# Kernel tuning notes

Hardware: AMD Instinct MI355X
Metric: run time of the kernel (lower is better)

The kernel has to match this reference:

```python
import jax, jax.numpy as jnp
import numpy as np

D_MODEL = 2048
N_HEADS = 16
HEAD_DIM = D_MODEL // N_HEADS  # 128
B, T = 2, 1024
XL_LEN = 1024


def setup_inputs() -> dict:
    key = jax.random.key(0)
    ks = jax.random.split(key, 8)
    # rotary angles for head_dim/2 pairs (llama-style)
    inv_freq = 1.0 / (10000.0 ** (jnp.arange(0, HEAD_DIM, 2, dtype=jnp.float32) / HEAD_DIM))
    t = jnp.arange(T, dtype=jnp.float32)
    freqs = jnp.outer(t, inv_freq)  # [T, HEAD_DIM//2]
    return {
        "x": jax.random.normal(ks[0], (B, T, D_MODEL), dtype=jnp.float32),
        "cos": jnp.cos(freqs),
        "sin": jnp.sin(freqs),
        "k_xl": jax.random.normal(ks[1], (B, XL_LEN, D_MODEL), dtype=jnp.float32),
        "v_xl": jax.random.normal(ks[2], (B, XL_LEN, D_MODEL), dtype=jnp.float32),
        "pos_emb": jax.random.normal(ks[3], (XL_LEN, D_MODEL), dtype=jnp.float32) * 0.02,
        "w_qkv": jax.random.normal(ks[4], (3 * D_MODEL, D_MODEL), dtype=jnp.float32) * 0.02,
        "w_proj": jax.random.normal(ks[5], (D_MODEL, D_MODEL), dtype=jnp.float32) * 0.02,
        "is_causal": 0,
    }


def _apply_rope(x, cos, sin):
    # x: [B, T, H, hd]; cos/sin: [T, hd//2]
    xr = x.reshape(*x.shape[:-1], HEAD_DIM // 2, 2)
    x1, x2 = xr[..., 0], xr[..., 1]
    c = cos[None, :, None, :]
    s = sin[None, :, None, :]
    o1 = x1 * c - x2 * s
    o2 = x1 * s + x2 * c
    return jnp.stack([o1, o2], axis=-1).reshape(x.shape)


def reference(x, cos, sin, k_xl, v_xl, pos_emb, w_qkv, w_proj, is_causal):
    Bq, Tq, C = x.shape
    H, hd = N_HEADS, HEAD_DIM
    qkv = jnp.einsum('btc,fc->btf', x, w_qkv)  # fused QKV projection
    q, k, v = jnp.split(qkv, 3, axis=-1)
    # add learned XL positional embedding to cached keys (self.k_xl += emb(arange))
    k_xl = k_xl + pos_emb[None, :, :]
    q = q.reshape(Bq, Tq, H, hd)
    k = k.reshape(Bq, -1, H, hd)
    v = v.reshape(Bq, -1, H, hd)
    q = _apply_rope(q, cos, sin)
    k = _apply_rope(k, cos, sin)
    q = q.transpose(0, 2, 1, 3)  # [B,H,T,hd]
    k = k.transpose(0, 2, 1, 3)
    v = v.transpose(0, 2, 1, 3)
    k_xl_h = k_xl.reshape(Bq, -1, H, hd).transpose(0, 2, 1, 3)
    v_xl_h = v_xl.reshape(Bq, -1, H, hd).transpose(0, 2, 1, 3)
    k_full = jnp.concatenate([k_xl_h, k], axis=-2)  # [B,H,XL+T,hd]
    v_full = jnp.concatenate([v_xl_h, v], axis=-2)
    scale = 1.0 / jnp.sqrt(jnp.asarray(hd, dtype=q.dtype))
    scores = jnp.einsum('bhqd,bhkd->bhqk', q, k_full) * scale
    if is_causal:
        Kv = k_full.shape[-2]
        qi = jnp.arange(Tq)[:, None]
        ki = jnp.arange(Kv)[None, :]
        scores = jnp.where(ki <= qi + (Kv - Tq), scores, jnp.finfo(scores.dtype).min)
    attn = jax.nn.softmax(scores, axis=-1)
    y = jnp.einsum('bhqk,bhkd->bhqd', attn, v_full)
    y = y.transpose(0, 2, 1, 3).reshape(Bq, Tq, C)
    return jnp.einsum('btc,oc->bto', y, w_proj)
```

## Files before the change

### kernel.cpp

```cpp
#include <hip/hip_runtime.h>
#include <stdint.h>

typedef unsigned short u16;
typedef __attribute__((ext_vector_type(4))) float f32x4;
typedef __attribute__((ext_vector_type(8))) short bf16x8;
typedef __attribute__((ext_vector_type(4))) uint32_t u32x4;

#define D_MODEL 2048
#define NHEADS 16
#define HD 128
#define BSZ 2
#define TQ 1024
#define XL 1024
#define KVLEN 2048

__device__ __forceinline__ float b2f(u16 u) {
  union { uint32_t i; float f; } x; x.i = ((uint32_t)u) << 16; return x.f;
}
__device__ __forceinline__ u16 f2b(float f) {
  union { float f; uint32_t i; } x; x.f = f;
  uint32_t r = x.i + 0x7FFFu + ((x.i >> 16) & 1u);
  return (u16)(r >> 16);
}

union U4 { u32x4 u; u16 s[8]; };

__device__ __forceinline__ void async_copy16(const u16* g, u16* l) {
  __builtin_amdgcn_global_load_lds((__attribute__((address_space(1))) void*)g,
                                   (__attribute__((address_space(3))) void*)l,
                                   16, 0, 0);
}

__device__ __forceinline__ float rmax16(float v) {
  v = fmaxf(v, __shfl_xor(v, 1));
  v = fmaxf(v, __shfl_xor(v, 2));
  v = fmaxf(v, __shfl_xor(v, 4));
  v = fmaxf(v, __shfl_xor(v, 8));
  return v;
}
__device__ __forceinline__ float rsum16(float v) {
  v += __shfl_xor(v, 1);
  v += __shfl_xor(v, 2);
  v += __shfl_xor(v, 4);
  v += __shfl_xor(v, 8);
  return v;
}

struct PrefF32 {
  f32x4 lo, hi;
  __device__ __forceinline__ void load(const float* base, size_t off) {
    lo = *(const f32x4*)(base + off);
    hi = *(const f32x4*)(base + off + 4);
  }
  __device__ __forceinline__ u32x4 pack() const {
    U4 o;
    o.s[0] = f2b(lo[0]); o.s[1] = f2b(lo[1]); o.s[2] = f2b(lo[2]); o.s[3] = f2b(lo[3]);
    o.s[4] = f2b(hi[0]); o.s[5] = f2b(hi[1]); o.s[6] = f2b(hi[2]); o.s[7] = f2b(hi[3]);
    return o.u;
  }
};

__global__ __launch_bounds__(256, 4) void cvt_bf16(
    const float* __restrict__ src, u16* __restrict__ dst)
{
  const size_t id = (size_t)blockIdx.x * 256 + threadIdx.x;
  PrefF32 p; p.load(src, id * 8);
  *(u32x4*)&dst[id * 8] = p.pack();
}

template <bool AF32, bool BF32, bool CSPLIT>
__global__ __launch_bounds__(256, 2) void gemm_bt(
    const void* __restrict__ Av, const void* __restrict__ Bv,
    void* __restrict__ C0, void* __restrict__ C1, void* __restrict__ C2,
    int M, int N, int K)
{
  __shared__ u16 sA[128 * 32];
  __shared__ u16 sB[128 * 32];
  const int tid  = threadIdx.x;
  const int lane = tid & 63;
  const int wave = tid >> 6;
  const int quad = lane >> 4;
  const int mcol = lane & 15;
  const int wm = (wave >> 1) * 64;
  const int wn = (wave & 1) * 64;
  const int bm = blockIdx.y * 128;
  const int bnE = blockIdx.x * 128;

  f32x4 acc[4][4] = {};

  const int c0 = tid, c1 = tid + 256;
  size_t a0 = (size_t)(bm + (c0 >> 2)) * K + (c0 & 3) * 8;
  size_t a1 = (size_t)(bm + (c1 >> 2)) * K + (c1 & 3) * 8;
  size_t b0 = (size_t)(bnE + (c0 >> 2)) * K + (c0 & 3) * 8;
  size_t b1 = (size_t)(bnE + (c1 >> 2)) * K + (c1 & 3) * 8;

  PrefF32 pa0, pa1, pb0, pb1;
  if (AF32) { pa0.load((const float*)Av, a0); pa1.load((const float*)Av, a1); }
  if (BF32) { pb0.load((const float*)Bv, b0); pb1.load((const float*)Bv, b1); }

  const int nk = K >> 5;
  for (int kk = 0; kk < nk; ++kk) {
    if (!AF32) {
      async_copy16((const u16*)Av + a0, &sA[c0 * 8]);
      async_copy16((const u16*)Av + a1, &sA[c1 * 8]);
      a0 += 32; a1 += 32;
    } else {
      *(u32x4*)&sA[c0 * 8] = pa0.pack();
      *(u32x4*)&sA[c1 * 8] = pa1.pack();
    }
    if (!BF32) {
      async_copy16((const u16*)Bv + b0, &sB[c0 * 8]);
      async_copy16((const u16*)Bv + b1, &sB[c1 * 8]);
      b0 += 32; b1 += 32;
    } else {
      *(u32x4*)&sB[c0 * 8] = pb0.pack();
      *(u32x4*)&sB[c1 * 8] = pb1.pack();
    }
    __syncthreads();
    if (kk + 1 < nk) {
      if (AF32) { a0 += 32; a1 += 32; pa0.load((const float*)Av, a0); pa1.load((const float*)Av, a1); }
      if (BF32) { b0 += 32; b1 += 32; pb0.load((const float*)Bv, b0); pb1.load((const float*)Bv, b1); }
    }
    bf16x8 af[4], bff[4];
#pragma unroll
    for (int i = 0; i < 4; ++i) {
      af[i]  = *(const bf16x8*)&sA[(wm + i * 16 + mcol) * 32 + quad * 8];
      bff[i] = *(const bf16x8*)&sB[(wn + i * 16 + mcol) * 32 + quad * 8];
    }
#pragma unroll
    for (int i = 0; i < 4; ++i)
#pragma unroll
      for (int j = 0; j < 4; ++j)
        acc[i][j] = __builtin_amdgcn_mfma_f32_16x16x32_bf16(af[i], bff[j], acc[i][j], 0, 0, 0);
    __syncthreads();
  }

  if (CSPLIT) {
    const int sel = bnE >> 11;
    u16* Cp = (u16*)(sel == 0 ? C0 : (sel == 1 ? C1 : C2));
    const int bnl = (bnE & 2047) + wn;
#pragma unroll
    for (int i = 0; i < 4; ++i)
#pragma unroll
      for (int r = 0; r < 4; ++r) {
        const size_t base = (size_t)(bm + wm + i * 16 + quad * 4 + r) * 2048 + bnl;
#pragma unroll
        for (int j = 0; j < 4; ++j)
          Cp[base + j * 16 + mcol] = f2b(acc[i][j][r]);
      }
  } else {
    float* Cp = (float*)C0;
#pragma unroll
    for (int i = 0; i < 4; ++i)
#pragma unroll
      for (int r = 0; r < 4; ++r) {
        const size_t base = (size_t)(bm + wm + i * 16 + quad * 4 + r) * N + bnE + wn;
#pragma unroll
        for (int j = 0; j < 4; ++j)
          Cp[base + j * 16 + mcol] = acc[i][j][r];
      }
  }
}

__global__ __launch_bounds__(256, 4) void prep_k(
    const float* __restrict__ kxl, const float* __restrict__ pos,
    const u16* __restrict__ kbuf, const float* __restrict__ cosw,
    const float* __restrict__ sinw, u16* __restrict__ kfull)
{
  const int id = blockIdx.x * 256 + threadIdx.x;
  const int dc = id & 15;
  const int kv = (id >> 4) & 2047;
  const int bh = id >> 15;
  const int b = bh >> 4, h = bh & 15;
  const int d0 = dc * 8;
  U4 o;
  if (kv < XL) {
    const float* kp = kxl + ((size_t)b * XL + kv) * D_MODEL + h * HD + d0;
    const float* pp = pos + (size_t)kv * D_MODEL + h * HD + d0;
    f32x4 kl = *(const f32x4*)kp, kh = *(const f32x4*)(kp + 4);
    f32x4 pl = *(const f32x4*)pp, ph = *(const f32x4*)(pp + 4);
#pragma unroll
    for (int p = 0; p < 4; ++p) {
      o.s[p]     = f2b(kl[p] + pl[p]);
      o.s[4 + p] = f2b(kh[p] + ph[p]);
    }
  } else {
    const int tq = kv - XL;
    U4 kv_;
    kv_.u = *(const u32x4*)(kbuf + ((size_t)b * TQ + tq) * D_MODEL + h * HD + d0);
    f32x4 cv = *(const f32x4*)(cosw + tq * 64 + (d0 >> 1));
    f32x4 sv = *(const f32x4*)(sinw + tq * 64 + (d0 >> 1));
#pragma unroll
    for (int p = 0; p < 4; ++p) {
      const float e = b2f(kv_.s[2 * p]), od = b2f(kv_.s[2 * p + 1]);
      o.s[2 * p]     = f2b(e * cv[p] - od * sv[p]);
      o.s[2 * p + 1] = f2b(e * sv[p] + od * cv[p]);
    }
  }
  *(u32x4*)&kfull[((size_t)bh * KVLEN + kv) * HD + d0] = o.u;
}

__global__ __launch_bounds__(256, 4) void transpose_v(
    const float* __restrict__ v_xl, const u16* __restrict__ vbuf, u16* __restrict__ vt)
{
  __shared__ u16 tile[64 * 72];
  const int tid = threadIdx.x;
  const int kv0 = blockIdx.x * 64;
  const int d0  = blockIdx.y * 64;
  const int bh  = blockIdx.z;
  const int b = bh >> 4, h = bh & 15;
#pragma unroll
  for (int j = 0; j < 2; ++j) {
    const int id = tid + 256 * j;
    const int kr = id >> 3, dq = (id & 7) * 8;
    const int kvg = kv0 + kr;
    if (kvg < XL) {
      const float* src = v_xl + ((size_t)b * XL + kvg) * D_MODEL + h * HD + d0 + dq;
      PrefF32 p; p.load(src, 0);
      *(u32x4*)&tile[kr * 72 + dq] = p.pack();
    } else {
      const u16* src = vbuf + ((size_t)b * TQ + (kvg - XL)) * D_MODEL + h * HD + d0 + dq;
      *(u32x4*)&tile[kr * 72 + dq] = *(const u32x4*)src;
    }
  }
  __syncthreads();
#pragma unroll
  for (int j = 0; j < 2; ++j) {
    const int id = tid + 256 * j;
    const int dr = id >> 3, kq = (id & 7) * 8;
    U4 ov;
#pragma unroll
    for (int i = 0; i < 8; ++i) ov.s[i] = tile[(kq + i) * 72 + dr];
    *(u32x4*)&vt[((size_t)bh * HD + d0 + dr) * KVLEN + kv0 + kq] = ov.u;
  }
}

#define LSTR 136

__global__ __launch_bounds__(256, 2) void attn(
    const u16* __restrict__ q, const u16* __restrict__ kfull,
    const u16* __restrict__ vt, const float* __restrict__ cosw,
    const float* __restrict__ sinw, const int* __restrict__ iscausal,
    u16* __restrict__ y)
{
  __shared__ u16 sK[128 * LSTR];
  __shared__ u16 sV[128 * LSTR];

  const int tid  = threadIdx.x;
  const int lane = tid & 63;
  const int w    = tid >> 6;
  const int quad = lane >> 4;
  const int mcol = lane & 15;
  const int qt = blockIdx.x;
  const int bh = blockIdx.y;
  const int b = bh >> 4, h = bh & 15;
  const int causal = *iscausal;
  const float SC = 0.08838834764831845f;

  bf16x8 qf[4];
  {
    const int trow = qt * 64 + w * 16 + mcol;
    const u16* qrow = q + ((size_t)b * TQ + trow) * D_MODEL + h * HD;
    const float* crow = cosw + trow * 64;
    const float* srow = sinw + trow * 64;
#pragma unroll
    for (int ks = 0; ks < 4; ++ks) {
      const int d0 = ks * 32 + quad * 8;
      U4 qv; qv.u = *(const u32x4*)(qrow + d0);
      f32x4 cv = *(const f32x4*)(crow + (d0 >> 1));
      f32x4 sv = *(const f32x4*)(srow + (d0 >> 1));
      bf16x8 dst;
#pragma unroll
      for (int p = 0; p < 4; ++p) {
        const float e = b2f(qv.s[2 * p]), o = b2f(qv.s[2 * p + 1]);
        dst[2 * p]     = (short)f2b(e * cv[p] - o * sv[p]);
        dst[2 * p + 1] = (short)f2b(e * sv[p] + o * cv[p]);
      }
      qf[ks] = dst;
    }
  }

  f32x4 oacc[8] = {};
  float mrun[4], lrun[4];
#pragma unroll
  for (int r = 0; r < 4; ++r) { mrun[r] = -3.0e38f; lrun[r] = 0.f; }

  for (int t16 = 0; t16 < 16; ++t16) {
    const int kv0 = t16 * 128;
    __syncthreads();

#pragma unroll
    for (int j = 0; j < 8; ++j) {
      const int id = tid + 256 * j;
      const int row = id >> 4, c8 = (id & 15) * 8;
      *(u32x4*)&sK[row * LSTR + c8] =
          *(const u32x4*)(kfull + ((size_t)bh * KVLEN + kv0 + row) * HD + c8);
    }
#pragma unroll
    for (int j = 0; j < 8; ++j) {
      const int id = tid + 256 * j;
      const int dr = id >> 4, c8 = (id & 15) * 8;
      *(u32x4*)&sV[dr * LSTR + c8] =
          *(const u32x4*)(vt + ((size_t)bh * HD + dr) * KVLEN + kv0 + c8);
    }
    __syncthreads();

    f32x4 s[8] = {};
#pragma unroll
    for (int ks = 0; ks < 4; ++ks) {
      const int cc = ks * 4 + quad;
#pragma unroll
      for (int nt = 0; nt < 8; ++nt) {
        bf16x8 kf = *(const bf16x8*)&sK[(nt * 16 + mcol) * LSTR + cc * 8];
        s[nt] = __builtin_amdgcn_mfma_f32_16x16x32_bf16(qf[ks], kf, s[nt], 0, 0, 0);
      }
    }
#pragma unroll
    for (int nt = 0; nt < 8; ++nt)
#pragma unroll
      for (int r = 0; r < 4; ++r) s[nt][r] *= SC;
    if (causal) {
#pragma unroll
      for (int r = 0; r < 4; ++r) {
        const int qi = qt * 64 + w * 16 + quad * 4 + r;
#pragma unroll
        for (int nt = 0; nt < 8; ++nt) {
          const int ki = kv0 + nt * 16 + mcol;
          if (ki > qi + (KVLEN - TQ)) s[nt][r] = -1.0e30f;
        }
      }
    }

#pragma unroll
    for (int r = 0; r < 4; ++r) {
      float tm = -3.0e38f;
#pragma unroll
      for (int nt = 0; nt < 8; ++nt) tm = fmaxf(tm, s[nt][r]);
      tm = rmax16(tm);
      const float mo = mrun[r];
      const float mn = fmaxf(mo, tm);
      mrun[r] = mn;
      const float al = __expf(mo - mn);
      float rs = 0.f;
#pragma unroll
      for (int nt = 0; nt < 8; ++nt) {
        const float p = __expf(s[nt][r] - mn);
        s[nt][r] = p;
        rs += p;
      }
      rs = rsum16(rs);
      lrun[r] = lrun[r] * al + rs;
#pragma unroll
      for (int nd = 0; nd < 8; ++nd) oacc[nd][r] *= al;
    }
    __syncthreads();

    u16* sPw = &sK[w * 16 * LSTR];
#pragma unroll
    for (int r = 0; r < 4; ++r) {
      const int row = quad * 4 + r;
#pragma unroll
      for (int nt = 0; nt < 8; ++nt)
        sPw[row * LSTR + nt * 16 + mcol] = f2b(s[nt][r]);
    }

#pragma unroll
    for (int ks = 0; ks < 4; ++ks) {
      const int cc = ks * 4 + quad;
      bf16x8 pa = *(const bf16x8*)&sPw[mcol * LSTR + cc * 8];
#pragma unroll
      for (int nd = 0; nd < 8; ++nd) {
        bf16x8 vf = *(const bf16x8*)&sV[(nd * 16 + mcol) * LSTR + cc * 8];
        oacc[nd] = __builtin_amdgcn_mfma_f32_16x16x32_bf16(pa, vf, oacc[nd], 0, 0, 0);
      }
    }
  }

#pragma unroll
  for (int r = 0; r < 4; ++r) {
    const int trow = qt * 64 + w * 16 + quad * 4 + r;
    const float inv = 1.0f / lrun[r];
    u16* yr = y + ((size_t)b * TQ + trow) * D_MODEL + h * HD;
#pragma unroll
    for (int nd = 0; nd < 8; ++nd)
      yr[nd * 16 + mcol] = f2b(oacc[nd][r] * inv);
  }
}

extern "C" void kernel_launch(void* const* d_in, const int* in_sizes, int n_in,
                              void* d_out, int out_size, void* d_ws, size_t ws_size,
                              hipStream_t stream) {
  const float* x      = (const float*)d_in[0];
  const float* cosw   = (const float*)d_in[1];
  const float* sinw   = (const float*)d_in[2];
  const float* k_xl   = (const float*)d_in[3];
  const float* v_xl   = (const float*)d_in[4];
  const float* pos    = (const float*)d_in[5];
  const float* w_qkv  = (const float*)d_in[6];
  const float* w_proj = (const float*)d_in[7];
  const int* isc      = (const int*)d_in[8];
  float* out = (float*)d_out;

  char* ws = (char*)d_ws;
  u16* qbuf  = (u16*)ws;
  u16* kbuf  = (u16*)(ws + (size_t)8388608);
  u16* vbuf  = (u16*)(ws + (size_t)16777216);
  u16* wqb   = (u16*)(ws + (size_t)25165824);
  u16* kfull = (u16*)(ws + (size_t)25165824);
  u16* vt    = (u16*)(ws + (size_t)41943040);
  u16* y_ws  = kbuf;

  cvt_bf16<<<6144, 256, 0, stream>>>(w_qkv, wqb);

  dim3 g1(48, 16);
  gemm_bt<true, false, true><<<g1, 256, 0, stream>>>(
      x, wqb, qbuf, kbuf, vbuf, 2048, 6144, 2048);

  prep_k<<<4096, 256, 0, stream>>>(k_xl, pos, kbuf, cosw, sinw, kfull);

  dim3 gt(KVLEN / 64, HD / 64, BSZ * NHEADS);
  transpose_v<<<gt, 256, 0, stream>>>(v_xl, vbuf, vt);

  dim3 ga(16, BSZ * NHEADS);
  attn<<<ga, 256, 0, stream>>>(qbuf, kfull, vt, cosw, sinw, isc, y_ws);

  dim3 g2(16, 16);
  gemm_bt<false, true, false><<<g2, 256, 0, stream>>>(
      y_ws, w_proj, out, nullptr, nullptr, 2048, 2048, 2048);
}
```

Measured before the change: 390.4 us.

## Pre-convert GEMM inputs to bf16, prefetch attention K/V tiles, fold scale into Q

x and w_proj are now converted to bf16 in separate kernels, so the GEMM template always uses async global-to-LDS copies instead of converting fp32 inside the main loop. The output projection uses a 64-wide N tile, doubling its grid to 512 blocks. In attention, the next K/V tile is loaded into registers while the current tile is computed, which overlaps global loads with MFMA work. The softmax scale is also folded into Q during the RoPE step rather than applied per score. This adds extra conversion kernels and memory traffic, plus register pressure from the prefetch buffers.

```diff
diff --git a/kernel.cpp b/kernel.cpp
--- a/kernel.cpp
+++ b/kernel.cpp
@@ -68,69 +68,52 @@
   *(u32x4*)&dst[id * 8] = p.pack();
 }
 
-template <bool AF32, bool BF32, bool CSPLIT>
+template <int BN, bool CSPLIT>
 __global__ __launch_bounds__(256, 2) void gemm_bt(
-    const void* __restrict__ Av, const void* __restrict__ Bv,
+    const u16* __restrict__ A, const u16* __restrict__ B,
     void* __restrict__ C0, void* __restrict__ C1, void* __restrict__ C2,
     int M, int N, int K)
 {
+  constexpr int JN = BN / 32;
   __shared__ u16 sA[128 * 32];
-  __shared__ u16 sB[128 * 32];
+  __shared__ u16 sB[BN * 32];
   const int tid  = threadIdx.x;
   const int lane = tid & 63;
   const int wave = tid >> 6;
   const int quad = lane >> 4;
   const int mcol = lane & 15;
   const int wm = (wave >> 1) * 64;
-  const int wn = (wave & 1) * 64;
+  const int wn = (wave & 1) * (BN / 2);
   const int bm = blockIdx.y * 128;
-  const int bnE = blockIdx.x * 128;
-
-  f32x4 acc[4][4] = {};
+  const int bnE = blockIdx.x * BN;
+
+  f32x4 acc[4][JN] = {};
 
   const int c0 = tid, c1 = tid + 256;
   size_t a0 = (size_t)(bm + (c0 >> 2)) * K + (c0 & 3) * 8;
   size_t a1 = (size_t)(bm + (c1 >> 2)) * K + (c1 & 3) * 8;
   size_t b0 = (size_t)(bnE + (c0 >> 2)) * K + (c0 & 3) * 8;
-  size_t b1 = (size_t)(bnE + (c1 >> 2)) * K + (c1 & 3) * 8;
-
-  PrefF32 pa0, pa1, pb0, pb1;
-  if (AF32) { pa0.load((const float*)Av, a0); pa1.load((const float*)Av, a1); }
-  if (BF32) { pb0.load((const float*)Bv, b0); pb1.load((const float*)Bv, b1); }
+  size_t b1 = (BN == 128) ? (size_t)(bnE + (c1 >> 2)) * K + (c1 & 3) * 8 : 0;
 
   const int nk = K >> 5;
   for (int kk = 0; kk < nk; ++kk) {
-    if (!AF32) {
-      async_copy16((const u16*)Av + a0, &sA[c0 * 8]);
-      async_copy16((const u16*)Av + a1, &sA[c1 * 8]);
-      a0 += 32; a1 += 32;
-    } else {
-      *(u32x4*)&sA[c0 * 8] = pa0.pack();
-      *(u32x4*)&sA[c1 * 8] = pa1.pack();
-    }
-    if (!BF32) {
-      async_copy16((const u16*)Bv + b0, &sB[c0 * 8]);
-      async_copy16((const u16*)Bv + b1, &sB[c1 * 8]);
-      b0 += 32; b1 += 32;
-    } else {
-      *(u32x4*)&sB[c0 * 8] = pb0.pack();
-      *(u32x4*)&sB[c1 * 8] = pb1.pack();
-    }
+    async_copy16(A + a0, &sA[c0 * 8]);
+    async_copy16(A + a1, &sA[c1 * 8]);
+    async_copy16(B + b0, &sB[c0 * 8]);
+    if (BN == 128) async_copy16(B + b1, &sB[c1 * 8]);
+    a0 += 32; a1 += 32; b0 += 32; b1 += 32;
     __syncthreads();
-    if (kk + 1 < nk) {
-      if (AF32) { a0 += 32; a1 += 32; pa0.load((const float*)Av, a0); pa1.load((const float*)Av, a1); }
-      if (BF32) { b0 += 32; b1 += 32; pb0.load((const float*)Bv, b0); pb1.load((const float*)Bv, b1); }
-    }
-    bf16x8 af[4], bff[4];
-#pragma unroll
-    for (int i = 0; i < 4; ++i) {
-      af[i]  = *(const bf16x8*)&sA[(wm + i * 16 + mcol) * 32 + quad * 8];
-      bff[i] = *(const bf16x8*)&sB[(wn + i * 16 + mcol) * 32 + quad * 8];
-    }
+    bf16x8 af[4], bff[JN];
 #pragma unroll
     for (int i = 0; i < 4; ++i)
-#pragma unroll
-      for (int j = 0; j < 4; ++j)
+      af[i] = *(const bf16x8*)&sA[(wm + i * 16 + mcol) * 32 + quad * 8];
+#pragma unroll
+    for (int j = 0; j < JN; ++j)
+      bff[j] = *(const bf16x8*)&sB[(wn + j * 16 + mcol) * 32 + quad * 8];
+#pragma unroll
+    for (int i = 0; i < 4; ++i)
+#pragma unroll
+      for (int j = 0; j < JN; ++j)
         acc[i][j] = __builtin_amdgcn_mfma_f32_16x16x32_bf16(af[i], bff[j], acc[i][j], 0, 0, 0);
     __syncthreads();
   }
@@ -145,7 +128,7 @@
       for (int r = 0; r < 4; ++r) {
         const size_t base = (size_t)(bm + wm + i * 16 + quad * 4 + r) * 2048 + bnl;
 #pragma unroll
-        for (int j = 0; j < 4; ++j)
+        for (int j = 0; j < JN; ++j)
           Cp[base + j * 16 + mcol] = f2b(acc[i][j][r]);
       }
   } else {
@@ -156,7 +139,7 @@
       for (int r = 0; r < 4; ++r) {
         const size_t base = (size_t)(bm + wm + i * 16 + quad * 4 + r) * N + bnE + wn;
 #pragma unroll
-        for (int j = 0; j < 4; ++j)
+        for (int j = 0; j < JN; ++j)
           Cp[base + j * 16 + mcol] = acc[i][j][r];
       }
   }
@@ -273,37 +256,46 @@
 #pragma unroll
       for (int p = 0; p < 4; ++p) {
         const float e = b2f(qv.s[2 * p]), o = b2f(qv.s[2 * p + 1]);
-        dst[2 * p]     = (short)f2b(e * cv[p] - o * sv[p]);
-        dst[2 * p + 1] = (short)f2b(e * sv[p] + o * cv[p]);
+        dst[2 * p]     = (short)f2b((e * cv[p] - o * sv[p]) * SC);
+        dst[2 * p + 1] = (short)f2b((e * sv[p] + o * cv[p]) * SC);
       }
       qf[ks] = dst;
     }
   }
+
+  const int srow = tid >> 4;
+  const int sc8 = (tid & 15) * 8;
+  const u16* kbase = kfull + (size_t)bh * KVLEN * HD;
+  const u16* vbase = vt + (size_t)bh * HD * KVLEN;
+
+  u32x4 kreg[8], vreg[8];
+#define LOADT(KV0)                                                          \
+  do {                                                                      \
+    _Pragma("unroll") for (int j = 0; j < 8; ++j) {                         \
+      const int rr = srow + 16 * j;                                         \
+      kreg[j] = *(const u32x4*)(kbase + ((size_t)(KV0) + rr) * HD + sc8);   \
+      vreg[j] = *(const u32x4*)(vbase + (size_t)rr * KVLEN + (KV0) + sc8);  \
+    }                                                                       \
+  } while (0)
 
   f32x4 oacc[8] = {};
   float mrun[4], lrun[4];
 #pragma unroll
   for (int r = 0; r < 4; ++r) { mrun[r] = -3.0e38f; lrun[r] = 0.f; }
 
+  LOADT(0);
   for (int t16 = 0; t16 < 16; ++t16) {
+    __syncthreads();
+#pragma unroll
+    for (int j = 0; j < 8; ++j) {
+      const int rr = srow + 16 * j;
+      *(u32x4*)&sK[rr * LSTR + sc8] = kreg[j];
+      *(u32x4*)&sV[rr * LSTR + sc8] = vreg[j];
+    }
+    __syncthreads();
+    if (t16 < 15) LOADT((t16 + 1) * 128);
+
     const int kv0 = t16 * 128;
-    __syncthreads();
-
-#pragma unroll
-    for (int j = 0; j < 8; ++j) {
-      const int id = tid + 256 * j;
-      const int row = id >> 4, c8 = (id & 15) * 8;
-      *(u32x4*)&sK[row * LSTR + c8] =
-          *(const u32x4*)(kfull + ((size_t)bh * KVLEN + kv0 + row) * HD + c8);
-    }
-#pragma unroll
-    for (int j = 0; j < 8; ++j) {
-      const int id = tid + 256 * j;
-      const int dr = id >> 4, c8 = (id & 15) * 8;
-      *(u32x4*)&sV[dr * LSTR + c8] =
-          *(const u32x4*)(vt + ((size_t)bh * HD + dr) * KVLEN + kv0 + c8);
-    }
-    __syncthreads();
 
     f32x4 s[8] = {};
 #pragma unroll
@@ -315,10 +307,6 @@
         s[nt] = __builtin_amdgcn_mfma_f32_16x16x32_bf16(qf[ks], kf, s[nt], 0, 0, 0);
       }
     }
-#pragma unroll
-    for (int nt = 0; nt < 8; ++nt)
-#pragma unroll
-      for (int r = 0; r < 4; ++r) s[nt][r] *= SC;
     if (causal) {
 #pragma unroll
       for (int r = 0; r < 4; ++r) {
@@ -375,6 +363,7 @@
       }
     }
   }
+#undef LOADT
 
 #pragma unroll
   for (int r = 0; r < 4; ++r) {
@@ -407,14 +396,16 @@
   u16* vbuf  = (u16*)(ws + (size_t)16777216);
   u16* wqb   = (u16*)(ws + (size_t)25165824);
   u16* kfull = (u16*)(ws + (size_t)25165824);
+  u16* wpb   = (u16*)(ws + (size_t)25165824);
   u16* vt    = (u16*)(ws + (size_t)41943040);
+  u16* xb    = (u16*)(ws + (size_t)50331648);
   u16* y_ws  = kbuf;
 
+  cvt_bf16<<<2048, 256, 0, stream>>>(x, xb);
   cvt_bf16<<<6144, 256, 0, stream>>>(w_qkv, wqb);
 
   dim3 g1(48, 16);
-  gemm_bt<true, false, true><<<g1, 256, 0, stream>>>(
-      x, wqb, qbuf, kbuf, vbuf, 2048, 6144, 2048);
+  gemm_bt<128, true><<<g1, 256, 0, stream>>>(xb, wqb, qbuf, kbuf, vbuf, 2048, 6144, 2048);
 
   prep_k<<<4096, 256, 0, stream>>>(k_xl, pos, kbuf, cosw, sinw, kfull);
 
@@ -424,7 +415,8 @@
   dim3 ga(16, BSZ * NHEADS);
   attn<<<ga, 256, 0, stream>>>(qbuf, kfull, vt, cosw, sinw, isc, y_ws);
 
-  dim3 g2(16, 16);
-  gemm_bt<false, true, false><<<g2, 256, 0, stream>>>(
-      y_ws, w_proj, out, nullptr, nullptr, 2048, 2048, 2048);
-}
+  cvt_bf16<<<2048, 256, 0, stream>>>(w_proj, wpb);
+
+  dim3 g2(32, 16);
+  gemm_bt<64, false><<<g2, 256, 0, stream>>>(y_ws, wpb, out, nullptr, nullptr, 2048, 2048, 2048);
+}
```

After: 350.6 us. 1.11x faster.
